# Optimization experiments

Measured on AMD Instinct MI355X. Metric: run time of the kernel, lower is better.

## Reference

```python
import jax, jax.numpy as jnp
import numpy as np
from jax import lax

C = 640          # channels (hard-coded in module: GrootV3DLayer(channels=640))
D_INNER = 1280   # 2*C expansion
D_STATE = 8
DT_RANK = 40     # C // 16
K_CONV = 4
B_, H_, W_ = 1, 48, 48


def setup_inputs() -> dict:
    key = jax.random.key(0)
    ks = jax.random.split(key, 8)
    s = 0.02
    x = jax.random.normal(ks[0], (B_, C, H_, W_), jnp.float32)
    y = jax.random.normal(ks[1], (B_, C, H_, W_), jnp.float32)
    ln_g = jnp.ones((C,), jnp.float32)
    ln_b = jnp.zeros((C,), jnp.float32)
    W_in = jax.random.normal(ks[2], (C, 2 * D_INNER), jnp.float32) * s
    conv_w = jax.random.normal(ks[3], (D_INNER, 1, K_CONV), jnp.float32) * s
    W_xproj = jax.random.normal(ks[4], (D_INNER, DT_RANK + 2 * D_STATE), jnp.float32) * s
    W_dt = jax.random.normal(ks[5], (DT_RANK, D_INNER), jnp.float32) * s
    dt_bias = jnp.full((D_INNER,), -2.0, jnp.float32)  # softplus(-2) ~ 0.127
    A_log = jnp.log(jnp.broadcast_to(jnp.arange(1, D_STATE + 1, dtype=jnp.float32), (D_INNER, D_STATE)))
    Dp = jnp.ones((D_INNER,), jnp.float32)
    W_out = jax.random.normal(ks[6], (D_INNER, C), jnp.float32) * s
    return dict(x=x, y=y, ln_g=ln_g, ln_b=ln_b, W_in=W_in, conv_w=conv_w,
                W_xproj=W_xproj, W_dt=W_dt, dt_bias=dt_bias, A_log=A_log, Dp=Dp, W_out=W_out)


def _layernorm(x, g, b):
    m = x.mean(-1, keepdims=True)
    v = jnp.mean((x - m) ** 2, axis=-1, keepdims=True)
    return (x - m) * lax.rsqrt(v + 1e-5) * g + b


def _grootv3d_layer(seq, ln_g, ln_b, W_in, conv_w, W_xproj, W_dt, dt_bias, A_log, Dp, W_out):
    # seq: (B, L, C) flattened spatial sequence; Mamba-style selective-scan block.
    xn = _layernorm(seq, ln_g, ln_b)
    xz = xn @ W_in                                # (B, L, 2*D_INNER)
    xp, z = jnp.split(xz, 2, axis=-1)
    # causal depthwise conv along sequence
    xc = lax.conv_general_dilated(
        xp.transpose(0, 2, 1), conv_w, (1,), [(K_CONV - 1, 0)],
        feature_group_count=D_INNER, dimension_numbers=('NCH', 'OIH', 'NCH')
    ).transpose(0, 2, 1)                          # (B, L, D_INNER)
    xa = jax.nn.silu(xc)
    proj = xa @ W_xproj                           # (B, L, DT_RANK + 2*D_STATE)
    dt = jax.nn.softplus(proj[..., :DT_RANK] @ W_dt + dt_bias)   # (B, L, D_INNER)
    Bm = proj[..., DT_RANK:DT_RANK + D_STATE]     # (B, L, D_STATE)
    Cm = proj[..., DT_RANK + D_STATE:]            # (B, L, D_STATE)
    A = -jnp.exp(A_log)                           # (D_INNER, D_STATE)
    dA = jnp.exp(dt[..., None] * A)               # (B, L, D_INNER, D_STATE)
    dBx = (dt * xa)[..., None] * Bm[:, :, None, :]

    def comb(e1, e2):
        a1, b1 = e1
        a2, b2 = e2
        return (a2 * a1, a2 * b1 + b2)

    _, h = lax.associative_scan(comb, (dA, dBx), axis=1)          # h: (B, L, D_INNER, D_STATE)
    y_ssm = jnp.einsum('blds,bls->bld', h, Cm) + xa * Dp
    yo = y_ssm * jax.nn.silu(z)
    return yo @ W_out + seq                       # residual


def reference(x, y, ln_g, ln_b, W_in, conv_w, W_xproj, W_dt, dt_bias, A_log, Dp, W_out):
    B, Cc, H, W = x.shape
    xy = jnp.concatenate([x, y], axis=-1)         # (B, C, H, 2W)
    t = xy.transpose(0, 2, 3, 1)                  # (B, H, 2W, C)  (channel_first=False)
    seq = t.reshape(B, H * 2 * W, Cc)
    out = _grootv3d_layer(seq, ln_g, ln_b, W_in, conv_w, W_xproj, W_dt, dt_bias, A_log, Dp, W_out)
    f2 = out.reshape(B, H, 2 * W, Cc).transpose(0, 3, 1, 2)       # (B, C, H, 2W)
    xf_sm = f2[..., :W]
    yf_sm = f2[..., W:]
    return (xf_sm, yf_sm)
```

## Files before the change

### kernel.cpp

```cpp
#include <hip/hip_runtime.h>
#include <hip/hip_bf16.h>
#include <math.h>

#define LSEQ 4608
#define CDIM 640
#define DIN 1280
#define DSTATE 8
#define DTRANK 40
#define NCHUNK 192
#define CLEN 24
#define OUT_HALF 1474560

typedef __attribute__((ext_vector_type(8))) short short8v;
typedef __attribute__((ext_vector_type(4))) float f32x4;

__device__ __forceinline__ float silu_f(float v){ return v / (1.f + __expf(-v)); }

__device__ __forceinline__ void gload16(const void* g, void* l){
    __builtin_amdgcn_global_load_lds((const __attribute__((address_space(1))) void*)g,
                                     (__attribute__((address_space(3))) void*)l, 16, 0, 0);
}

__global__ __launch_bounds__(256) void k_transpose(const float* __restrict__ in,
        __hip_bfloat16* __restrict__ out, int R, int C, int Cp, int Rp)
{
    __shared__ float t[32][33];
    int tid = threadIdx.x;
    int tx = tid & 31, ty = tid >> 5;
    int r0 = blockIdx.y*32, c0 = blockIdx.x*32;
    #pragma unroll
    for (int i = 0; i < 4; ++i){
        int r = r0 + ty + i*8, c = c0 + tx;
        t[ty + i*8][tx] = (r < R && c < C) ? in[(size_t)r*C + c] : 0.f;
    }
    __syncthreads();
    #pragma unroll
    for (int i = 0; i < 4; ++i){
        int c = c0 + ty + i*8;
        out[(size_t)c*Rp + r0 + tx] = __float2bfloat16(t[tx][ty + i*8]);
    }
}

__global__ __launch_bounds__(256) void k_gather(const float* __restrict__ x,
        const float* __restrict__ y, float* __restrict__ seq)
{
    __shared__ float t[32][33];
    int tid = threadIdx.x;
    int tx = tid & 31, ty = tid >> 5;
    int l0 = blockIdx.x*32, c0 = blockIdx.y*32;
    int l = l0 + tx;
    int h = l / 96, w2 = l - h*96;
    const float* src = (w2 < 48) ? x : y;
    int col = h*48 + (w2 < 48 ? w2 : w2 - 48);
    #pragma unroll
    for (int i = 0; i < 4; ++i)
        t[tx][ty + i*8] = src[(size_t)(c0 + ty + i*8)*2304 + col];
    __syncthreads();
    #pragma unroll
    for (int i = 0; i < 4; ++i){
        int l2 = l0 + ty + i*8;
        seq[(size_t)l2*640 + c0 + tx] = t[ty + i*8][tx];
    }
}

__global__ __launch_bounds__(64) void k_ln(const float* __restrict__ seq,
        const float* __restrict__ g, const float* __restrict__ bta,
        __hip_bfloat16* __restrict__ xn)
{
    int l = blockIdx.x;
    int lane = threadIdx.x;
    const float* row = seq + (size_t)l*640;
    float2 v[5];
    float s = 0.f, s2 = 0.f;
    #pragma unroll
    for (int j = 0; j < 5; ++j){
        v[j] = *(const float2*)&row[j*128 + lane*2];
        s  += v[j].x + v[j].y;
        s2 += v[j].x*v[j].x + v[j].y*v[j].y;
    }
    #pragma unroll
    for (int off = 32; off > 0; off >>= 1){
        s  += __shfl_xor(s,  off, 64);
        s2 += __shfl_xor(s2, off, 64);
    }
    float mean = s * (1.f/640.f);
    float rs = rsqrtf(s2 * (1.f/640.f) - mean*mean + 1e-5f);
    #pragma unroll
    for (int j = 0; j < 5; ++j){
        int c = j*128 + lane*2;
        float2 gg = *(const float2*)&g[c];
        float2 bb = *(const float2*)&bta[c];
        __hip_bfloat162 ob;
        ob.x = __float2bfloat16((v[j].x - mean)*rs*gg.x + bb.x);
        ob.y = __float2bfloat16((v[j].y - mean)*rs*gg.y + bb.y);
        *(__hip_bfloat162*)&xn[(size_t)l*640 + c] = ob;
    }
}

template<int EPI, int BN>
__global__ __launch_bounds__(256) void gemm_mfma(const __hip_bfloat16* __restrict__ A,
        const __hip_bfloat16* __restrict__ Bt, float* __restrict__ C,
        const float* __restrict__ aux, float* __restrict__ outp, int N, int K)
{
    constexpr int NF = BN/32;
    __shared__ __align__(16) short As[128*32];
    __shared__ __align__(16) short Bs[BN*32];
    int tid = threadIdx.x;
    int lane = tid & 63, wid = tid >> 6;
    int bn0 = blockIdx.x*BN, bm0 = blockIdx.y*128;
    int wm = wid >> 1, wn = wid & 1;
    int fr = lane & 15, ko = (lane >> 4) << 3;
    f32x4 acc[4][NF];
    #pragma unroll
    for (int m = 0; m < 4; ++m)
    #pragma unroll
    for (int n = 0; n < NF; ++n)
        acc[m][n] = (f32x4){0.f, 0.f, 0.f, 0.f};

    for (int k0 = 0; k0 < K; k0 += 32){
        #pragma unroll
        for (int i = 0; i < 2; ++i){
            int c = tid + 256*i;
            int row = c >> 2, kq = (c & 3) << 3;
            gload16(&A[(size_t)(bm0 + row)*K + k0 + kq], (char*)As + c*16);
        }
        #pragma unroll
        for (int i = 0; i < BN/64; ++i){
            int c = tid + 256*i;
            int row = c >> 2, kq = (c & 3) << 3;
            gload16(&Bt[(size_t)(bn0 + row)*K + k0 + kq], (char*)Bs + c*16);
        }
        __syncthreads();
        short8v a[4], b[NF];
        #pragma unroll
        for (int m = 0; m < 4; ++m) a[m] = *(const short8v*)&As[(wm*64 + m*16 + fr)*32 + ko];
        #pragma unroll
        for (int n = 0; n < NF; ++n) b[n] = *(const short8v*)&Bs[(wn*(BN/2) + n*16 + fr)*32 + ko];
        #pragma unroll
        for (int m = 0; m < 4; ++m)
        #pragma unroll
        for (int n = 0; n < NF; ++n)
            acc[m][n] = __builtin_amdgcn_mfma_f32_16x16x32_bf16(a[m], b[n], acc[m][n], 0, 0, 0);
        __syncthreads();
    }

    int rq = (lane >> 4) * 4;
    #pragma unroll
    for (int m = 0; m < 4; ++m){
        #pragma unroll
        for (int r = 0; r < 4; ++r){
            int row = bm0 + wm*64 + m*16 + rq + r;
            if (EPI == 1){
                int hh = row / 96, w2 = row - hh*96;
                int obase = (w2 < 48) ? (hh*48 + w2) : (OUT_HALF + hh*48 + w2 - 48);
                #pragma unroll
                for (int n = 0; n < NF; ++n){
                    int col = bn0 + wn*(BN/2) + n*16 + fr;
                    float v = acc[m][n][r] + aux[(size_t)row*N + col];
                    outp[obase + (size_t)col*2304] = v;
                }
            } else {
                #pragma unroll
                for (int n = 0; n < NF; ++n){
                    int col = bn0 + wn*(BN/2) + n*16 + fr;
                    float v = acc[m][n][r];
                    if (EPI == 2){
                        v += aux[col];
                        v = (v > 20.f) ? v : log1pf(__expf(v));
                    }
                    C[(size_t)row*N + col] = v;
                }
            }
        }
    }
}

__global__ __launch_bounds__(256) void xproj_mfma(const __hip_bfloat16* __restrict__ A,
        const __hip_bfloat16* __restrict__ Bt, float* __restrict__ proj,
        __hip_bfloat16* __restrict__ projb)
{
    __shared__ __align__(16) short As[128*32];
    __shared__ __align__(16) short Bs[64*32];
    int tid = threadIdx.x;
    int lane = tid & 63, wid = tid >> 6;
    int bm0 = blockIdx.x*128;
    int fr = lane & 15, ko = (lane >> 4) << 3;
    f32x4 acc[2][4];
    #pragma unroll
    for (int m = 0; m < 2; ++m)
    #pragma unroll
    for (int n = 0; n < 4; ++n)
        acc[m][n] = (f32x4){0.f, 0.f, 0.f, 0.f};

    for (int k0 = 0; k0 < 1280; k0 += 32){
        #pragma unroll
        for (int i = 0; i < 2; ++i){
            int c = tid + 256*i;
            int row = c >> 2, kq = (c & 3) << 3;
            gload16(&A[(size_t)(bm0 + row)*1280 + k0 + kq], (char*)As + c*16);
        }
        {
            int c = tid;
            int row = c >> 2, kq = (c & 3) << 3;
            gload16(&Bt[(size_t)row*1280 + k0 + kq], (char*)Bs + c*16);
        }
        __syncthreads();
        short8v a[2], b[4];
        #pragma unroll
        for (int m = 0; m < 2; ++m) a[m] = *(const short8v*)&As[(wid*32 + m*16 + fr)*32 + ko];
        #pragma unroll
        for (int n = 0; n < 4; ++n) b[n] = *(const short8v*)&Bs[(n*16 + fr)*32 + ko];
        #pragma unroll
        for (int m = 0; m < 2; ++m)
        #pragma unroll
        for (int n = 0; n < 4; ++n)
            acc[m][n] = __builtin_amdgcn_mfma_f32_16x16x32_bf16(a[m], b[n], acc[m][n], 0, 0, 0);
        __syncthreads();
    }
    int rq = (lane >> 4) * 4;
    #pragma unroll
    for (int m = 0; m < 2; ++m)
    #pragma unroll
    for (int r = 0; r < 4; ++r){
        int row = bm0 + wid*32 + m*16 + rq + r;
        #pragma unroll
        for (int n = 0; n < 4; ++n){
            int col = n*16 + fr;
            float v = acc[m][n][r];
            if (col < 56) proj[row*56 + col] = v;
            projb[row*64 + col] = __float2bfloat16(col < 40 ? v : 0.f);
        }
    }
}

__global__ __launch_bounds__(256) void k_conv(const float* __restrict__ xz, const float* __restrict__ cw,
        float* __restrict__ xa, __hip_bfloat16* __restrict__ xab)
{
    int gid = blockIdx.x*256 + threadIdx.x;
    int l = gid / 1280, d = gid - l*1280;
    float4 w = *(const float4*)&cw[d*4];
    float acc = w.w * xz[l*2560 + d];
    if (l >= 1) acc = fmaf(w.z, xz[(l-1)*2560 + d], acc);
    if (l >= 2) acc = fmaf(w.y, xz[(l-2)*2560 + d], acc);
    if (l >= 3) acc = fmaf(w.x, xz[(l-3)*2560 + d], acc);
    float v = silu_f(acc);
    xa[gid] = v;
    xab[gid] = __float2bfloat16(v);
}

__global__ __launch_bounds__(256) void k_scan1(const float* __restrict__ dt, const float* __restrict__ xa,
        const float* __restrict__ proj, const float* __restrict__ A_log,
        float* __restrict__ Hc, float* __restrict__ Sdt)
{
    __shared__ float Bsh[CLEN*8];
    int tid = threadIdx.x;
    int c = blockIdx.x;
    int d = blockIdx.y*256 + tid;
    if (tid < CLEN*8){
        int ll = tid >> 3, s = tid & 7;
        Bsh[tid] = proj[(c*CLEN + ll)*56 + 40 + s];
    }
    float As[8];
    #pragma unroll
    for (int s = 0; s < 8; ++s) As[s] = -__expf(A_log[d*8 + s]);
    __syncthreads();
    float h[8] = {};
    float sdt = 0.f;
    #pragma unroll 4
    for (int ll = 0; ll < CLEN; ++ll){
        int l = c*CLEN + ll;
        float dtv = dt[l*1280 + d];
        float xav = xa[l*1280 + d];
        sdt += dtv;
        float dx = dtv * xav;
        #pragma unroll
        for (int s = 0; s < 8; ++s)
            h[s] = fmaf(__expf(dtv*As[s]), h[s], dx * Bsh[ll*8 + s]);
    }
    int base = (c*1280 + d)*8;
    #pragma unroll
    for (int s = 0; s < 8; ++s) Hc[base + s] = h[s];
    Sdt[c*1280 + d] = sdt;
}

__global__ __launch_bounds__(256) void k_scan2(const float* __restrict__ A_log, const float* __restrict__ Hc,
        const float* __restrict__ Sdt, float* __restrict__ Hinit)
{
    int gid = blockIdx.x*256 + threadIdx.x;
    int d = gid >> 3;
    float As = -__expf(A_log[gid]);
    float h = 0.f;
    #pragma unroll 4
    for (int c = 0; c < NCHUNK; ++c){
        Hinit[c*10240 + gid] = h;
        float sdt = Sdt[c*1280 + d];
        h = fmaf(__expf(sdt*As), h, Hc[c*10240 + gid]);
    }
}

__global__ __launch_bounds__(256) void k_scan3(const float* __restrict__ dt, const float* __restrict__ xa,
        const float* __restrict__ proj, const float* __restrict__ xz, const float* __restrict__ A_log,
        const float* __restrict__ Dp, const float* __restrict__ Hinit, __hip_bfloat16* __restrict__ yo)
{
    __shared__ float Bsh[CLEN*8];
    __shared__ float Csh[CLEN*8];
    int tid = threadIdx.x;
    int c = blockIdx.x;
    int d = blockIdx.y*256 + tid;
    if (tid < CLEN*8){
        int ll = tid >> 3, s = tid & 7;
        Bsh[tid] = proj[(c*CLEN + ll)*56 + 40 + s];
        Csh[tid] = proj[(c*CLEN + ll)*56 + 48 + s];
    }
    float As[8];
    #pragma unroll
    for (int s = 0; s < 8; ++s) As[s] = -__expf(A_log[d*8 + s]);
    float Dpv = Dp[d];
    __syncthreads();
    float h[8];
    int hbase = (c*1280 + d)*8;
    #pragma unroll
    for (int s = 0; s < 8; ++s) h[s] = Hinit[hbase + s];
    #pragma unroll 4
    for (int ll = 0; ll < CLEN; ++ll){
        int l = c*CLEN + ll;
        float dtv = dt[l*1280 + d];
        float xav = xa[l*1280 + d];
        float dx = dtv * xav;
        float yv = 0.f;
        #pragma unroll
        for (int s = 0; s < 8; ++s){
            h[s] = fmaf(__expf(dtv*As[s]), h[s], dx * Bsh[ll*8 + s]);
            yv = fmaf(h[s], Csh[ll*8 + s], yv);
        }
        yv = fmaf(xav, Dpv, yv);
        float zv = xz[l*2560 + 1280 + d];
        yo[l*1280 + d] = __float2bfloat16(yv * silu_f(zv));
    }
}

extern "C" void kernel_launch(void* const* d_in, const int* in_sizes, int n_in,
                              void* d_out, int out_size, void* d_ws, size_t ws_size,
                              hipStream_t stream) {
    const float* x       = (const float*)d_in[0];
    const float* y       = (const float*)d_in[1];
    const float* ln_g    = (const float*)d_in[2];
    const float* ln_b    = (const float*)d_in[3];
    const float* W_in    = (const float*)d_in[4];
    const float* conv_w  = (const float*)d_in[5];
    const float* W_xproj = (const float*)d_in[6];
    const float* W_dt    = (const float*)d_in[7];
    const float* dt_bias = (const float*)d_in[8];
    const float* A_log   = (const float*)d_in[9];
    const float* Dp      = (const float*)d_in[10];
    const float* W_out   = (const float*)d_in[11];
    float* out = (float*)d_out;
    char* w = (char*)d_ws;

    float* seq   = (float*)(w);
    float* xz    = (float*)(w + 11796480);
    float* xa    = (float*)(w + 58982400);
    float* proj  = (float*)(w + 82575360);
    float* dt    = (float*)(w + 83607552);
    float* Hc    = (float*)(w + 107200512);
    float* Sdt   = (float*)(w + 115064832);
    float* Hinit = (float*)(w + 116047872);
    __hip_bfloat16* xnb   = (__hip_bfloat16*)(w + 123912192);
    __hip_bfloat16* xab   = (__hip_bfloat16*)(w + 129810432);
    __hip_bfloat16* yob   = (__hip_bfloat16*)(w + 141606912);
    __hip_bfloat16* WtIn  = (__hip_bfloat16*)(w + 153403392);
    __hip_bfloat16* WtOut = (__hip_bfloat16*)(w + 156680192);
    __hip_bfloat16* WtXp  = (__hip_bfloat16*)(w + 158318592);
    __hip_bfloat16* projb = (__hip_bfloat16*)(w + 158482432);
    __hip_bfloat16* Wdtb  = (__hip_bfloat16*)(w + 159072256);

    k_transpose<<<dim3(80, 20), 256, 0, stream>>>(W_in,    WtIn,  640, 2560, 2560, 640);
    k_transpose<<<dim3(20, 40), 256, 0, stream>>>(W_out,   WtOut, 1280, 640, 640, 1280);
    k_transpose<<<dim3(2,  40), 256, 0, stream>>>(W_xproj, WtXp,  1280, 56,  64, 1280);
    k_transpose<<<dim3(40,  2), 256, 0, stream>>>(W_dt,    Wdtb,  40, 1280, 1280, 64);

    k_gather<<<dim3(144, 20), 256, 0, stream>>>(x, y, seq);
    k_ln<<<LSEQ, 64, 0, stream>>>(seq, ln_g, ln_b, xnb);
    gemm_mfma<0,128><<<dim3(20, 36), 256, 0, stream>>>(xnb, WtIn, xz, nullptr, nullptr, 2560, 640);
    k_conv<<<(LSEQ*DIN)/256, 256, 0, stream>>>(xz, conv_w, xa, xab);
    xproj_mfma<<<36, 256, 0, stream>>>(xab, WtXp, proj, projb);
    gemm_mfma<2,128><<<dim3(10, 36), 256, 0, stream>>>(projb, Wdtb, dt, dt_bias, nullptr, 1280, 64);
    k_scan1<<<dim3(NCHUNK, 5), 256, 0, stream>>>(dt, xa, proj, A_log, Hc, Sdt);
    k_scan2<<<40, 256, 0, stream>>>(A_log, Hc, Sdt, Hinit);
    k_scan3<<<dim3(NCHUNK, 5), 256, 0, stream>>>(dt, xa, proj, xz, A_log, Dp, Hinit, yob);
    gemm_mfma<1,64><<<dim3(10, 36), 256, 0, stream>>>(yob, WtOut, nullptr, seq, out, 640, 1280);
}
```

Measured before the change: 323.5 us.

## Store xz, xa and dt intermediates in bf16 and process two channels per scan thread

The in-projection and dt GEMMs now write bf16 outputs instead of fp32. The conv and both scan kernels read the bf16 xz, xa and dt arrays and handle two channels per thread with paired loads and vector stores of the chunk states. The four weight-transpose launches are merged into one kernel. The goal is to roughly halve the memory traffic of the elementwise and scan stages and to cut launch overhead. The cost is lower precision in the scan inputs and in the gate z, and fewer threads per scan block.

```diff
diff --git a/kernel.cpp b/kernel.cpp
--- a/kernel.cpp
+++ b/kernel.cpp
@@ -21,13 +21,23 @@
                                      (__attribute__((address_space(3))) void*)l, 16, 0, 0);
 }
 
-__global__ __launch_bounds__(256) void k_transpose(const float* __restrict__ in,
-        __hip_bfloat16* __restrict__ out, int R, int C, int Cp, int Rp)
+__global__ __launch_bounds__(256) void k_transpose_all(
+        const float* __restrict__ W_in, const float* __restrict__ W_out,
+        const float* __restrict__ W_xp, const float* __restrict__ W_dt,
+        __hip_bfloat16* __restrict__ WtIn, __hip_bfloat16* __restrict__ WtOut,
+        __hip_bfloat16* __restrict__ WtXp, __hip_bfloat16* __restrict__ Wdtb)
 {
     __shared__ float t[32][33];
+    int b = blockIdx.x;
+    const float* in; __hip_bfloat16* out; int R, C, Cp, Rp, nbx;
+    if (b < 1600)      { in = W_in;  out = WtIn;  R = 640;  C = 2560; Cp = 2560; Rp = 640;  nbx = 80; }
+    else if (b < 2400) { b -= 1600; in = W_out; out = WtOut; R = 1280; C = 640;  Cp = 640;  Rp = 1280; nbx = 20; }
+    else if (b < 2480) { b -= 2400; in = W_xp;  out = WtXp;  R = 1280; C = 56;   Cp = 64;   Rp = 1280; nbx = 2; }
+    else               { b -= 2480; in = W_dt;  out = Wdtb;  R = 40;   C = 1280; Cp = 1280; Rp = 64;   nbx = 40; }
+    int bx = b % nbx, by = b / nbx;
     int tid = threadIdx.x;
     int tx = tid & 31, ty = tid >> 5;
-    int r0 = blockIdx.y*32, c0 = blockIdx.x*32;
+    int r0 = by*32, c0 = bx*32;
     #pragma unroll
     for (int i = 0; i < 4; ++i){
         int r = r0 + ty + i*8, c = c0 + tx;
@@ -99,7 +109,7 @@
 
 template<int EPI, int BN>
 __global__ __launch_bounds__(256) void gemm_mfma(const __hip_bfloat16* __restrict__ A,
-        const __hip_bfloat16* __restrict__ Bt, float* __restrict__ C,
+        const __hip_bfloat16* __restrict__ Bt, __hip_bfloat16* __restrict__ Cb,
         const float* __restrict__ aux, float* __restrict__ outp, int N, int K)
 {
     constexpr int NF = BN/32;
@@ -168,7 +178,7 @@
                         v += aux[col];
                         v = (v > 20.f) ? v : log1pf(__expf(v));
                     }
-                    C[(size_t)row*N + col] = v;
+                    Cb[(size_t)row*N + col] = __float2bfloat16(v);
                 }
             }
         }
@@ -233,54 +243,82 @@
     }
 }
 
-__global__ __launch_bounds__(256) void k_conv(const float* __restrict__ xz, const float* __restrict__ cw,
-        float* __restrict__ xa, __hip_bfloat16* __restrict__ xab)
+__global__ __launch_bounds__(256) void k_conv(const __hip_bfloat16* __restrict__ xzb,
+        const float* __restrict__ cw, __hip_bfloat16* __restrict__ xab)
 {
     int gid = blockIdx.x*256 + threadIdx.x;
-    int l = gid / 1280, d = gid - l*1280;
-    float4 w = *(const float4*)&cw[d*4];
-    float acc = w.w * xz[l*2560 + d];
-    if (l >= 1) acc = fmaf(w.z, xz[(l-1)*2560 + d], acc);
-    if (l >= 2) acc = fmaf(w.y, xz[(l-2)*2560 + d], acc);
-    if (l >= 3) acc = fmaf(w.x, xz[(l-3)*2560 + d], acc);
-    float v = silu_f(acc);
-    xa[gid] = v;
-    xab[gid] = __float2bfloat16(v);
-}
-
-__global__ __launch_bounds__(256) void k_scan1(const float* __restrict__ dt, const float* __restrict__ xa,
-        const float* __restrict__ proj, const float* __restrict__ A_log,
-        float* __restrict__ Hc, float* __restrict__ Sdt)
+    int l = gid / 640, dp = gid - l*640;
+    int d = dp*2;
+    float4 w0 = *(const float4*)&cw[d*4];
+    float4 w1 = *(const float4*)&cw[d*4 + 4];
+    __hip_bfloat162 v = *(const __hip_bfloat162*)&xzb[(size_t)l*2560 + d];
+    float a0 = w0.w * __bfloat162float(v.x);
+    float a1 = w1.w * __bfloat162float(v.y);
+    if (l >= 1){
+        v = *(const __hip_bfloat162*)&xzb[(size_t)(l-1)*2560 + d];
+        a0 = fmaf(w0.z, __bfloat162float(v.x), a0);
+        a1 = fmaf(w1.z, __bfloat162float(v.y), a1);
+    }
+    if (l >= 2){
+        v = *(const __hip_bfloat162*)&xzb[(size_t)(l-2)*2560 + d];
+        a0 = fmaf(w0.y, __bfloat162float(v.x), a0);
+        a1 = fmaf(w1.y, __bfloat162float(v.y), a1);
+    }
+    if (l >= 3){
+        v = *(const __hip_bfloat162*)&xzb[(size_t)(l-3)*2560 + d];
+        a0 = fmaf(w0.x, __bfloat162float(v.x), a0);
+        a1 = fmaf(w1.x, __bfloat162float(v.y), a1);
+    }
+    __hip_bfloat162 o;
+    o.x = __float2bfloat16(silu_f(a0));
+    o.y = __float2bfloat16(silu_f(a1));
+    *(__hip_bfloat162*)&xab[(size_t)l*1280 + d] = o;
+}
+
+__global__ __launch_bounds__(128) void k_scan1(const __hip_bfloat16* __restrict__ dtb,
+        const __hip_bfloat16* __restrict__ xab, const float* __restrict__ proj,
+        const float* __restrict__ A_log, float* __restrict__ Hc, float* __restrict__ Sdt)
 {
     __shared__ float Bsh[CLEN*8];
     int tid = threadIdx.x;
     int c = blockIdx.x;
-    int d = blockIdx.y*256 + tid;
-    if (tid < CLEN*8){
-        int ll = tid >> 3, s = tid & 7;
-        Bsh[tid] = proj[(c*CLEN + ll)*56 + 40 + s];
-    }
-    float As[8];
-    #pragma unroll
-    for (int s = 0; s < 8; ++s) As[s] = -__expf(A_log[d*8 + s]);
+    int d = blockIdx.y*256 + tid*2;
+    for (int i = tid; i < CLEN*8; i += 128){
+        int ll = i >> 3, s = i & 7;
+        Bsh[i] = proj[(c*CLEN + ll)*56 + 40 + s];
+    }
+    float As0[8], As1[8];
+    #pragma unroll
+    for (int s = 0; s < 8; ++s){
+        As0[s] = -__expf(A_log[d*8 + s]);
+        As1[s] = -__expf(A_log[d*8 + 8 + s]);
+    }
     __syncthreads();
-    float h[8] = {};
-    float sdt = 0.f;
+    float h0[8] = {}, h1[8] = {};
+    float sdt0 = 0.f, sdt1 = 0.f;
     #pragma unroll 4
     for (int ll = 0; ll < CLEN; ++ll){
         int l = c*CLEN + ll;
-        float dtv = dt[l*1280 + d];
-        float xav = xa[l*1280 + d];
-        sdt += dtv;
-        float dx = dtv * xav;
-        #pragma unroll
-        for (int s = 0; s < 8; ++s)
-            h[s] = fmaf(__expf(dtv*As[s]), h[s], dx * Bsh[ll*8 + s]);
-    }
-    int base = (c*1280 + d)*8;
-    #pragma unroll
-    for (int s = 0; s < 8; ++s) Hc[base + s] = h[s];
-    Sdt[c*1280 + d] = sdt;
+        __hip_bfloat162 dt2 = *(const __hip_bfloat162*)&dtb[(size_t)l*1280 + d];
+        __hip_bfloat162 xa2 = *(const __hip_bfloat162*)&xab[(size_t)l*1280 + d];
+        float dtv0 = __bfloat162float(dt2.x), dtv1 = __bfloat162float(dt2.y);
+        float dx0 = dtv0 * __bfloat162float(xa2.x);
+        float dx1 = dtv1 * __bfloat162float(xa2.y);
+        sdt0 += dtv0; sdt1 += dtv1;
+        #pragma unroll
+        for (int s = 0; s < 8; ++s){
+            float bb = Bsh[ll*8 + s];
+            h0[s] = fmaf(__expf(dtv0*As0[s]), h0[s], dx0 * bb);
+            h1[s] = fmaf(__expf(dtv1*As1[s]), h1[s], dx1 * bb);
+        }
+    }
+    size_t base = ((size_t)c*1280 + d)*8;
+    *(float4*)&Hc[base     ] = make_float4(h0[0], h0[1], h0[2], h0[3]);
+    *(float4*)&Hc[base + 4 ] = make_float4(h0[4], h0[5], h0[6], h0[7]);
+    *(float4*)&Hc[base + 8 ] = make_float4(h1[0], h1[1], h1[2], h1[3]);
+    *(float4*)&Hc[base + 12] = make_float4(h1[4], h1[5], h1[6], h1[7]);
+    Sdt[c*1280 + d] = sdt0;
+    Sdt[c*1280 + d + 1] = sdt1;
 }
 
 __global__ __launch_bounds__(256) void k_scan2(const float* __restrict__ A_log, const float* __restrict__ Hc,
@@ -298,44 +336,69 @@
     }
 }
 
-__global__ __launch_bounds__(256) void k_scan3(const float* __restrict__ dt, const float* __restrict__ xa,
-        const float* __restrict__ proj, const float* __restrict__ xz, const float* __restrict__ A_log,
-        const float* __restrict__ Dp, const float* __restrict__ Hinit, __hip_bfloat16* __restrict__ yo)
+__global__ __launch_bounds__(128) void k_scan3(const __hip_bfloat16* __restrict__ dtb,
+        const __hip_bfloat16* __restrict__ xab, const float* __restrict__ proj,
+        const __hip_bfloat16* __restrict__ xzb, const float* __restrict__ A_log,
+        const float* __restrict__ Dp, const float* __restrict__ Hinit,
+        __hip_bfloat16* __restrict__ yo)
 {
     __shared__ float Bsh[CLEN*8];
     __shared__ float Csh[CLEN*8];
     int tid = threadIdx.x;
     int c = blockIdx.x;
-    int d = blockIdx.y*256 + tid;
-    if (tid < CLEN*8){
-        int ll = tid >> 3, s = tid & 7;
-        Bsh[tid] = proj[(c*CLEN + ll)*56 + 40 + s];
-        Csh[tid] = proj[(c*CLEN + ll)*56 + 48 + s];
-    }
-    float As[8];
-    #pragma unroll
-    for (int s = 0; s < 8; ++s) As[s] = -__expf(A_log[d*8 + s]);
-    float Dpv = Dp[d];
+    int d = blockIdx.y*256 + tid*2;
+    for (int i = tid; i < CLEN*8; i += 128){
+        int ll = i >> 3, s = i & 7;
+        Bsh[i] = proj[(c*CLEN + ll)*56 + 40 + s];
+        Csh[i] = proj[(c*CLEN + ll)*56 + 48 + s];
+    }
+    float As0[8], As1[8];
+    #pragma unroll
+    for (int s = 0; s < 8; ++s){
+        As0[s] = -__expf(A_log[d*8 + s]);
+        As1[s] = -__expf(A_log[d*8 + 8 + s]);
+    }
+    float Dp0 = Dp[d], Dp1 = Dp[d + 1];
     __syncthreads();
-    float h[8];
-    int hbase = (c*1280 + d)*8;
-    #pragma unroll
-    for (int s = 0; s < 8; ++s) h[s] = Hinit[hbase + s];
+    float h0[8], h1[8];
+    size_t base = ((size_t)c*1280 + d)*8;
+    {
+        float4 t0 = *(const float4*)&Hinit[base];
+        float4 t1 = *(const float4*)&Hinit[base + 4];
+        float4 t2 = *(const float4*)&Hinit[base + 8];
+        float4 t3 = *(const float4*)&Hinit[base + 12];
+        h0[0]=t0.x; h0[1]=t0.y; h0[2]=t0.z; h0[3]=t0.w;
+        h0[4]=t1.x; h0[5]=t1.y; h0[6]=t1.z; h0[7]=t1.w;
+        h1[0]=t2.x; h1[1]=t2.y; h1[2]=t2.z; h1[3]=t2.w;
+        h1[4]=t3.x; h1[5]=t3.y; h1[6]=t3.z; h1[7]=t3.w;
+    }
     #pragma unroll 4
     for (int ll = 0; ll < CLEN; ++ll){
         int l = c*CLEN + ll;
-        float dtv = dt[l*1280 + d];
-        float xav = xa[l*1280 + d];
-        float dx = dtv * xav;
-        float yv = 0.f;
+        __hip_bfloat162 dt2 = *(const __hip_bfloat162*)&dtb[(size_t)l*1280 + d];
+        __hip_bfloat162 xa2 = *(const __hip_bfloat162*)&xab[(size_t)l*1280 + d];
+        __hip_bfloat162 z2  = *(const __hip_bfloat162*)&xzb[(size_t)l*2560 + 1280 + d];
+        float dtv0 = __bfloat162float(dt2.x), dtv1 = __bfloat162float(dt2.y);
+        float xav0 = __bfloat162float(xa2.x), xav1 = __bfloat162float(xa2.y);
+        float dx0 = dtv0 * xav0, dx1 = dtv1 * xav1;
+        float yv0 = 0.f, yv1 = 0.f;
         #pragma unroll
         for (int s = 0; s < 8; ++s){
-            h[s] = fmaf(__expf(dtv*As[s]), h[s], dx * Bsh[ll*8 + s]);
-            yv = fmaf(h[s], Csh[ll*8 + s], yv);
-        }
-        yv = fmaf(xav, Dpv, yv);
-        float zv = xz[l*2560 + 1280 + d];
-        yo[l*1280 + d] = __float2bfloat16(yv * silu_f(zv));
+            float bb = Bsh[ll*8 + s];
+            float cc = Csh[ll*8 + s];
+            h0[s] = fmaf(__expf(dtv0*As0[s]), h0[s], dx0 * bb);
+            h1[s] = fmaf(__expf(dtv1*As1[s]), h1[s], dx1 * bb);
+            yv0 = fmaf(h0[s], cc, yv0);
+            yv1 = fmaf(h1[s], cc, yv1);
+        }
+        yv0 = fmaf(xav0, Dp0, yv0);
+        yv1 = fmaf(xav1, Dp1, yv1);
+        yv0 *= silu_f(__bfloat162float(z2.x));
+        yv1 *= silu_f(__bfloat162float(z2.y));
+        __hip_bfloat162 o;
+        o.x = __float2bfloat16(yv0);
+        o.y = __float2bfloat16(yv1);
+        *(__hip_bfloat162*)&yo[(size_t)l*1280 + d] = o;
     }
 }
 
@@ -357,36 +420,32 @@
     float* out = (float*)d_out;
     char* w = (char*)d_ws;
 
-    float* seq   = (float*)(w);
-    float* xz    = (float*)(w + 11796480);
-    float* xa    = (float*)(w + 58982400);
-    float* proj  = (float*)(w + 82575360);
-    float* dt    = (float*)(w + 83607552);
-    float* Hc    = (float*)(w + 107200512);
-    float* Sdt   = (float*)(w + 115064832);
-    float* Hinit = (float*)(w + 116047872);
-    __hip_bfloat16* xnb   = (__hip_bfloat16*)(w + 123912192);
-    __hip_bfloat16* xab   = (__hip_bfloat16*)(w + 129810432);
-    __hip_bfloat16* yob   = (__hip_bfloat16*)(w + 141606912);
-    __hip_bfloat16* WtIn  = (__hip_bfloat16*)(w + 153403392);
-    __hip_bfloat16* WtOut = (__hip_bfloat16*)(w + 156680192);
-    __hip_bfloat16* WtXp  = (__hip_bfloat16*)(w + 158318592);
-    __hip_bfloat16* projb = (__hip_bfloat16*)(w + 158482432);
-    __hip_bfloat16* Wdtb  = (__hip_bfloat16*)(w + 159072256);
-
-    k_transpose<<<dim3(80, 20), 256, 0, stream>>>(W_in,    WtIn,  640, 2560, 2560, 640);
-    k_transpose<<<dim3(20, 40), 256, 0, stream>>>(W_out,   WtOut, 1280, 640, 640, 1280);
-    k_transpose<<<dim3(2,  40), 256, 0, stream>>>(W_xproj, WtXp,  1280, 56,  64, 1280);
-    k_transpose<<<dim3(40,  2), 256, 0, stream>>>(W_dt,    Wdtb,  40, 1280, 1280, 64);
-
+    float*          seq   = (float*)(w);
+    __hip_bfloat16* xzb   = (__hip_bfloat16*)(w + 11796480);
+    __hip_bfloat16* xab   = (__hip_bfloat16*)(w + 35389440);
+    __hip_bfloat16* dtb   = (__hip_bfloat16*)(w + 47185920);
+    float*          proj  = (float*)(w + 58982400);
+    __hip_bfloat16* projb = (__hip_bfloat16*)(w + 60014592);
+    float*          Hc    = (float*)(w + 60604416);
+    float*          Sdt   = (float*)(w + 68468736);
+    float*          Hinit = (float*)(w + 69451776);
+    __hip_bfloat16* xnb   = (__hip_bfloat16*)(w + 77316096);
+    __hip_bfloat16* yob   = (__hip_bfloat16*)(w + 83214336);
+    __hip_bfloat16* WtIn  = (__hip_bfloat16*)(w + 95010816);
+    __hip_bfloat16* WtOut = (__hip_bfloat16*)(w + 98287616);
+    __hip_bfloat16* WtXp  = (__hip_bfloat16*)(w + 99926016);
+    __hip_bfloat16* Wdtb  = (__hip_bfloat16*)(w + 100089856);
+
+    k_transpose_all<<<2560, 256, 0, stream>>>(W_in, W_out, W_xproj, W_dt,
+                                              WtIn, WtOut, WtXp, Wdtb);
     k_gather<<<dim3(144, 20), 256, 0, stream>>>(x, y, seq);
     k_ln<<<LSEQ, 64, 0, stream>>>(seq, ln_g, ln_b, xnb);
-    gemm_mfma<0,128><<<dim3(20, 36), 256, 0, stream>>>(xnb, WtIn, xz, nullptr, nullptr, 2560, 640);
-    k_conv<<<(LSEQ*DIN)/256, 256, 0, stream>>>(xz, conv_w, xa, xab);
+    gemm_mfma<0,128><<<dim3(20, 36), 256, 0, stream>>>(xnb, WtIn, xzb, nullptr, nullptr, 2560, 640);
+    k_conv<<<(LSEQ*640)/256, 256, 0, stream>>>(xzb, conv_w, xab);
     xproj_mfma<<<36, 256, 0, stream>>>(xab, WtXp, proj, projb);
-    gemm_mfma<2,128><<<dim3(10, 36), 256, 0, stream>>>(projb, Wdtb, dt, dt_bias, nullptr, 1280, 64);
-    k_scan1<<<dim3(NCHUNK, 5), 256, 0, stream>>>(dt, xa, proj, A_log, Hc, Sdt);
+    gemm_mfma<2,128><<<dim3(10, 36), 256, 0, stream>>>(projb, Wdtb, dtb, dt_bias, nullptr, 1280, 64);
+    k_scan1<<<dim3(NCHUNK, 5), 128, 0, stream>>>(dtb, xab, proj, A_log, Hc, Sdt);
     k_scan2<<<40, 256, 0, stream>>>(A_log, Hc, Sdt, Hinit);
-    k_scan3<<<dim3(NCHUNK, 5), 256, 0, stream>>>(dt, xa, proj, xz, A_log, Dp, Hinit, yob);
+    k_scan3<<<dim3(NCHUNK, 5), 128, 0, stream>>>(dtb, xab, proj, xzb, A_log, Dp, Hinit, yob);
     gemm_mfma<1,64><<<dim3(10, 36), 256, 0, stream>>>(yob, WtOut, nullptr, seq, out, 640, 1280);
 }
```

Measured after the change: 318.1 us. No clear change (-1.7%).
